# Kernel tuning notes

Hardware: AMD Instinct MI355X
Metric: run time of the kernel (lower is better)

The kernel has to match this reference:

```python
import jax, jax.numpy as jnp
import numpy as np

EPS = 1e-5  # eqx.nn.LayerNorm default


def _layer_norm(x, w, b):
    m = x.mean(-1, keepdims=True)
    v = ((x - m) ** 2).mean(-1, keepdims=True)
    return (x - m) / jnp.sqrt(v + EPS) * w + b


def _s4_block(x, nw, nb, lre, lim, bre, bim, cre, cim, d, lstep, ow, ob, o2w, o2b):
    # x: [L, H]. One SequenceBlock: LayerNorm -> S4 recurrence (lax.scan) -> GELU -> GLU-style gated linear -> residual.
    skip = x
    h = _layer_norm(x, nw, nb)
    Lam = lre + 1j * lim                      # [H, N] complex diagonal state matrix
    step = jnp.exp(lstep)[:, None]            # [H, 1] per-channel timescale
    BL = 1.0 / (1.0 - (step / 2.0) * Lam)     # bilinear discretization
    Abar = BL * (1.0 + (step / 2.0) * Lam)    # [H, N]
    Bbar = BL * step * (bre + 1j * bim)       # [H, N]
    C = cre + 1j * cim                        # [H, N]

    def scan_fn(state, u):                    # state: [H, N] complex, u: [H]
        new = Abar * state + Bbar * u[:, None]
        y = 2.0 * jnp.sum(C * new, axis=-1).real + d * u
        return new, y

    init = jnp.zeros(Abar.shape, Abar.dtype)  # cell.init_state
    _, y = jax.lax.scan(scan_fn, init, h)     # [L, H]
    y = jax.nn.gelu(y)
    y = (y @ ow.T + ob) * jax.nn.sigmoid(y @ o2w.T + o2b)
    return skip + y


def setup_inputs() -> dict:
    key = jax.random.key(0)
    L, IN, OUT, H, N, NL = 2048, 4, 3, 512, 32, 4
    ks = jax.random.split(key, 16)
    return {
        "x": jax.random.normal(ks[0], (L, IN), jnp.float32),
        "enc_w": jax.random.normal(ks[1], (H, IN), jnp.float32) / np.sqrt(IN),
        "enc_b": jnp.zeros((H,), jnp.float32),
        "dec_w": jax.random.normal(ks[2], (OUT, H), jnp.float32) / np.sqrt(H),
        "dec_b": jnp.zeros((OUT,), jnp.float32),
        "norm_w": jnp.ones((NL, H), jnp.float32),
        "norm_b": jnp.zeros((NL, H), jnp.float32),
        "lam_re": -0.5 - jax.random.uniform(ks[3], (NL, H, N), jnp.float32),  # stable (Re < 0)
        "lam_im": np.pi * jax.random.normal(ks[4], (NL, H, N), jnp.float32),
        "b_re": jax.random.normal(ks[5], (NL, H, N), jnp.float32) / np.sqrt(N),
        "b_im": jax.random.normal(ks[6], (NL, H, N), jnp.float32) / np.sqrt(N),
        "c_re": jax.random.normal(ks[7], (NL, H, N), jnp.float32) / np.sqrt(N),
        "c_im": jax.random.normal(ks[8], (NL, H, N), jnp.float32) / np.sqrt(N),
        "d": jax.random.normal(ks[9], (NL, H), jnp.float32),
        "log_step": float(np.log(1e-3)) + float(np.log(1e-1) - np.log(1e-3)) * jax.random.uniform(ks[10], (NL, H), jnp.float32),
        "out_w": jax.random.normal(ks[11], (NL, H, H), jnp.float32) / np.sqrt(H),
        "out_b": jnp.zeros((NL, H), jnp.float32),
        "out2_w": jax.random.normal(ks[12], (NL, H, H), jnp.float32) / np.sqrt(H),
        "out2_b": jnp.zeros((NL, H), jnp.float32),
    }


def reference(x, enc_w, enc_b, dec_w, dec_b, norm_w, norm_b, lam_re, lam_im, b_re, b_im, c_re, c_im, d, log_step, out_w, out_b, out2_w, out2_b):
    h = x @ enc_w.T + enc_b                   # encoder: [L, IN] -> [L, H]
    for i in range(norm_w.shape[0]):          # fixed small n_layers loop
        h = _s4_block(h, norm_w[i], norm_b[i], lam_re[i], lam_im[i], b_re[i], b_im[i],
                      c_re[i], c_im[i], d[i], log_step[i], out_w[i], out_b[i], out2_w[i], out2_b[i])
    return h @ dec_w.T + dec_b                # decoder: [L, H] -> [L, OUT]
```

## Files before the change

### kernel.cpp

```cpp
#include <hip/hip_runtime.h>
#include <hip/hip_bf16.h>
#include <math.h>

#define LSEQ 2048
#define HD   512
#define NST  32
#define LC   64
#define NCHK 32
#define HH   (HD * HD)

typedef __bf16 bf16;
typedef __bf16 bf16x8 __attribute__((ext_vector_type(8)));
typedef float  floatx4 __attribute__((ext_vector_type(4)));

__device__ __forceinline__ float wave_reduce_add(float v) {
#pragma unroll
    for (int m = 32; m; m >>= 1) v += __shfl_xor(v, m, 64);
    return v;
}

__device__ __forceinline__ float gelu_tanh(float x) {
    float z = 0.7978845608028654f * (x + 0.044715f * x * x * x);
    float e = __expf(2.f * z);
    float th = 1.f - 2.f / (e + 1.f);
    return 0.5f * x * (1.f + th);
}

__device__ __forceinline__ void make_ab(float lre, float lim, float step,
                                        float br0, float bi0,
                                        float& ar, float& ai, float& br, float& bi) {
    float s2 = 0.5f * step;
    float dr = 1.f - s2 * lre, di = -s2 * lim;
    float inv = 1.f / (dr * dr + di * di);
    float blr = dr * inv, bli = -di * inv;
    float nr = 1.f + s2 * lre, ni = s2 * lim;
    ar = blr * nr - bli * ni;
    ai = blr * ni + bli * nr;
    float tr = step * br0, ti = step * bi0;
    br = blr * tr - bli * ti;
    bi = blr * ti + bli * tr;
}

__global__ __launch_bounds__(256) void cvt_kernel(
    const float* __restrict__ ow, const float* __restrict__ o2w,
    bf16* __restrict__ wb) {
    const float* src = blockIdx.y ? o2w : ow;
    bf16* dst = wb + blockIdx.y * (4 * HH);
    int i = (blockIdx.x * 256 + threadIdx.x) * 8;
    float4 a = *(const float4*)(src + i);
    float4 b = *(const float4*)(src + i + 4);
    bf16x8 o;
    o[0] = (bf16)a.x; o[1] = (bf16)a.y; o[2] = (bf16)a.z; o[3] = (bf16)a.w;
    o[4] = (bf16)b.x; o[5] = (bf16)b.y; o[6] = (bf16)b.z; o[7] = (bf16)b.w;
    *(bf16x8*)(dst + i) = o;
}

__global__ __launch_bounds__(256) void enc_kernel(
    const float* __restrict__ x, const float* __restrict__ w,
    const float* __restrict__ b, float* __restrict__ h) {
    int idx = blockIdx.x * 256 + threadIdx.x;
    int t = idx >> 9, i = idx & (HD - 1);
    float acc = b[i];
    float4 xv = *(const float4*)(x + t * 4);
    float4 wv = *(const float4*)(w + i * 4);
    acc = fmaf(xv.x, wv.x, acc);
    acc = fmaf(xv.y, wv.y, acc);
    acc = fmaf(xv.z, wv.z, acc);
    acc = fmaf(xv.w, wv.w, acc);
    h[idx] = acc;
}

__global__ __launch_bounds__(256) void ln_kernel(
    const float* __restrict__ h, float* __restrict__ hn,
    const float* __restrict__ w, const float* __restrict__ b) {
    int wv = threadIdx.x >> 6, lane = threadIdx.x & 63;
    int row = blockIdx.x * 4 + wv;
    const float* hp = h + row * HD + lane * 8;
    float v[8];
    *(float4*)(v)     = *(const float4*)(hp);
    *(float4*)(v + 4) = *(const float4*)(hp + 4);
    float s = 0.f;
#pragma unroll
    for (int e = 0; e < 8; ++e) s += v[e];
    s = wave_reduce_add(s);
    float m = s * (1.f / HD);
    float q = 0.f;
#pragma unroll
    for (int e = 0; e < 8; ++e) { float d = v[e] - m; q += d * d; }
    q = wave_reduce_add(q);
    float rstd = rsqrtf(q * (1.f / HD) + 1e-5f);
    float w8[8], b8[8];
    *(float4*)(w8)     = *(const float4*)(w + lane * 8);
    *(float4*)(w8 + 4) = *(const float4*)(w + lane * 8 + 4);
    *(float4*)(b8)     = *(const float4*)(b + lane * 8);
    *(float4*)(b8 + 4) = *(const float4*)(b + lane * 8 + 4);
    float o[8];
#pragma unroll
    for (int e = 0; e < 8; ++e)
        o[e] = (v[e] - m) * rstd * w8[e] + b8[e];
    float* op = hn + row * HD + lane * 8;
    *(float4*)op       = *(float4*)o;
    *(float4*)(op + 4) = *(float4*)(o + 4);
}

__global__ __launch_bounds__(256) void p1_kernel(
    const float* __restrict__ u,
    const float* __restrict__ lre_p, const float* __restrict__ lim_p,
    const float* __restrict__ bre_p, const float* __restrict__ bim_p,
    const float* __restrict__ lstep_p,
    float2* __restrict__ f) {
    int ch = blockIdx.x * 32 + (threadIdx.x >> 3);
    int sub = threadIdx.x & 7;
    int chunk = blockIdx.y;
    float step = __expf(lstep_p[ch]);
    float ar[4], ai[4], br[4], bi[4], sr[4] = {0,0,0,0}, si[4] = {0,0,0,0};
#pragma unroll
    for (int j = 0; j < 4; ++j) {
        int idx = ch * NST + sub + 8 * j;
        make_ab(lre_p[idx], lim_p[idx], step,
                bre_p[idx], bim_p[idx], ar[j], ai[j], br[j], bi[j]);
    }
    const float* up = u + chunk * LC * HD + ch;
#pragma unroll 4
    for (int t = 0; t < LC; ++t) {
        float uu = up[t * HD];
#pragma unroll
        for (int j = 0; j < 4; ++j) {
            float nr = fmaf(ar[j], sr[j], fmaf(-ai[j], si[j], br[j] * uu));
            float ni = fmaf(ai[j], sr[j], fmaf( ar[j], si[j], bi[j] * uu));
            sr[j] = nr; si[j] = ni;
        }
    }
#pragma unroll
    for (int j = 0; j < 4; ++j)
        f[(chunk * HD + ch) * NST + sub + 8 * j] = make_float2(sr[j], si[j]);
}

__global__ __launch_bounds__(256) void p3_kernel(
    const float* __restrict__ u, const float2* __restrict__ f,
    const float* __restrict__ lre_p, const float* __restrict__ lim_p,
    const float* __restrict__ bre_p, const float* __restrict__ bim_p,
    const float* __restrict__ cre_p, const float* __restrict__ cim_p,
    const float* __restrict__ d_p,   const float* __restrict__ lstep_p,
    bf16* __restrict__ g) {
    int ch = blockIdx.x * 32 + (threadIdx.x >> 3);
    int sub = threadIdx.x & 7;
    int chunk = blockIdx.y;
    float step = __expf(lstep_p[ch]);
    float dch = d_p[ch];
    float ar[4], ai[4], br[4], bi[4], cr[4], ci[4];
#pragma unroll
    for (int j = 0; j < 4; ++j) {
        int idx = ch * NST + sub + 8 * j;
        make_ab(lre_p[idx], lim_p[idx], step,
                bre_p[idx], bim_p[idx], ar[j], ai[j], br[j], bi[j]);
        cr[j] = cre_p[idx];
        ci[j] = cim_p[idx];
    }
    float pr[4], pi[4];
#pragma unroll
    for (int j = 0; j < 4; ++j) {
        float xr = ar[j], xi = ai[j];
#pragma unroll
        for (int q = 0; q < 6; ++q) { float tt = xr * xr - xi * xi; xi = 2.f * xr * xi; xr = tt; }
        pr[j] = xr; pi[j] = xi;
    }
    float sr[4] = {0,0,0,0}, si[4] = {0,0,0,0};
    for (int c = 0; c < chunk; ++c) {
#pragma unroll
        for (int j = 0; j < 4; ++j) {
            float2 fv = f[(c * HD + ch) * NST + sub + 8 * j];
            float nr = fmaf(pr[j], sr[j], fmaf(-pi[j], si[j], fv.x));
            float ni = fmaf(pi[j], sr[j], fmaf( pr[j], si[j], fv.y));
            sr[j] = nr; si[j] = ni;
        }
    }
    const float* up = u + chunk * LC * HD + ch;
    bf16* gp = g + chunk * LC * HD + ch;
#pragma unroll 4
    for (int t = 0; t < LC; ++t) {
        float uu = up[t * HD];
        float p = 0.f;
#pragma unroll
        for (int j = 0; j < 4; ++j) {
            float nr = fmaf(ar[j], sr[j], fmaf(-ai[j], si[j], br[j] * uu));
            float ni = fmaf(ai[j], sr[j], fmaf( ar[j], si[j], bi[j] * uu));
            sr[j] = nr; si[j] = ni;
            p = fmaf(cr[j], nr, fmaf(-ci[j], ni, p));
        }
        p += __shfl_xor(p, 1);
        p += __shfl_xor(p, 2);
        p += __shfl_xor(p, 4);
        if (sub == 0) {
            float y = fmaf(dch, uu, 2.f * p);
            gp[t * HD] = (bf16)gelu_tanh(y);
        }
    }
}

__global__ __launch_bounds__(256) void mm_kernel(
    const bf16* __restrict__ A,
    const bf16* __restrict__ W1,
    const bf16* __restrict__ W2,
    const float* __restrict__ bias1, const float* __restrict__ bias2,
    float* __restrict__ Hio) {
    const int w = threadIdx.x >> 6, lane = threadIdx.x & 63;
    const int wm = w >> 1, wn = w & 1;
    const int mBase = blockIdx.y * 64 + wm * 32;
    const int nBase = blockIdx.x * 64 + wn * 32;
    const int lrow = lane & 15, quad = lane >> 4;

    floatx4 acc1[2][2] = {{{0.f,0.f,0.f,0.f},{0.f,0.f,0.f,0.f}},{{0.f,0.f,0.f,0.f},{0.f,0.f,0.f,0.f}}};
    floatx4 acc2[2][2] = {{{0.f,0.f,0.f,0.f},{0.f,0.f,0.f,0.f}},{{0.f,0.f,0.f,0.f},{0.f,0.f,0.f,0.f}}};

    for (int k0 = 0; k0 < HD; k0 += 32) {
        int kk = k0 + quad * 8;
        bf16x8 a0 = *(const bf16x8*)(A + (mBase + lrow) * HD + kk);
        bf16x8 a1 = *(const bf16x8*)(A + (mBase + 16 + lrow) * HD + kk);
        bf16x8 p0 = *(const bf16x8*)(W1 + (nBase + lrow) * HD + kk);
        bf16x8 p1 = *(const bf16x8*)(W1 + (nBase + 16 + lrow) * HD + kk);
        bf16x8 q0 = *(const bf16x8*)(W2 + (nBase + lrow) * HD + kk);
        bf16x8 q1 = *(const bf16x8*)(W2 + (nBase + 16 + lrow) * HD + kk);
        acc1[0][0] = __builtin_amdgcn_mfma_f32_16x16x32_bf16(a0, p0, acc1[0][0], 0, 0, 0);
        acc1[0][1] = __builtin_amdgcn_mfma_f32_16x16x32_bf16(a0, p1, acc1[0][1], 0, 0, 0);
        acc1[1][0] = __builtin_amdgcn_mfma_f32_16x16x32_bf16(a1, p0, acc1[1][0], 0, 0, 0);
        acc1[1][1] = __builtin_amdgcn_mfma_f32_16x16x32_bf16(a1, p1, acc1[1][1], 0, 0, 0);
        acc2[0][0] = __builtin_amdgcn_mfma_f32_16x16x32_bf16(a0, q0, acc2[0][0], 0, 0, 0);
        acc2[0][1] = __builtin_amdgcn_mfma_f32_16x16x32_bf16(a0, q1, acc2[0][1], 0, 0, 0);
        acc2[1][0] = __builtin_amdgcn_mfma_f32_16x16x32_bf16(a1, q0, acc2[1][0], 0, 0, 0);
        acc2[1][1] = __builtin_amdgcn_mfma_f32_16x16x32_bf16(a1, q1, acc2[1][1], 0, 0, 0);
    }

#pragma unroll
    for (int fm = 0; fm < 2; ++fm)
#pragma unroll
        for (int fn = 0; fn < 2; ++fn) {
            int j = nBase + fn * 16 + lrow;
            float bb1 = bias1[j], bb2 = bias2[j];
#pragma unroll
            for (int r = 0; r < 4; ++r) {
                int t = mBase + fm * 16 + quad * 4 + r;
                float z1 = acc1[fm][fn][r] + bb1;
                float z2 = acc2[fm][fn][r] + bb2;
                float val = z1 / (1.f + __expf(-z2));
                Hio[t * HD + j] += val;
            }
        }
}

__global__ __launch_bounds__(192) void dec_kernel(
    const float* __restrict__ h, const float* __restrict__ w,
    const float* __restrict__ b, float* __restrict__ out) {
    int j = threadIdx.x >> 6, lane = threadIdx.x & 63;
    int t = blockIdx.x;
    const float* hp = h + t * HD + lane * 8;
    float v[8];
    *(float4*)(v)     = *(const float4*)(hp);
    *(float4*)(v + 4) = *(const float4*)(hp + 4);
    float w8[8];
    *(float4*)(w8)     = *(const float4*)(w + j * HD + lane * 8);
    *(float4*)(w8 + 4) = *(const float4*)(w + j * HD + lane * 8 + 4);
    float s = 0.f;
#pragma unroll
    for (int e = 0; e < 8; ++e) s = fmaf(v[e], w8[e], s);
    s = wave_reduce_add(s);
    if (lane == 0) out[t * 3 + j] = s + b[j];
}

extern "C" void kernel_launch(void* const* d_in, const int* in_sizes, int n_in,
                              void* d_out, int out_size, void* d_ws, size_t ws_size,
                              hipStream_t stream) {
    const float* x   = (const float*)d_in[0];
    const float* ew  = (const float*)d_in[1];
    const float* eb  = (const float*)d_in[2];
    const float* dw  = (const float*)d_in[3];
    const float* db  = (const float*)d_in[4];
    const float* nw  = (const float*)d_in[5];
    const float* nb  = (const float*)d_in[6];
    const float* lre = (const float*)d_in[7];
    const float* lim = (const float*)d_in[8];
    const float* bre = (const float*)d_in[9];
    const float* bim = (const float*)d_in[10];
    const float* cre = (const float*)d_in[11];
    const float* cim = (const float*)d_in[12];
    const float* dd  = (const float*)d_in[13];
    const float* ls  = (const float*)d_in[14];
    const float* ow  = (const float*)d_in[15];
    const float* ob  = (const float*)d_in[16];
    const float* o2w = (const float*)d_in[17];
    const float* o2b = (const float*)d_in[18];

    char* ws = (char*)d_ws;
    float*  h  = (float*)ws;
    float*  hn = (float*)(ws + (4 << 20));
    float2* f  = (float2*)(ws + (8 << 20));
    bf16*   g  = (bf16*)(ws + (12 << 20));
    bf16*   wb = (bf16*)(ws + (14 << 20));

    cvt_kernel<<<dim3(4 * HH / (256 * 8), 2), 256, 0, stream>>>(ow, o2w, wb);
    enc_kernel<<<LSEQ * HD / 256, 256, 0, stream>>>(x, ew, eb, h);
    for (int lay = 0; lay < 4; ++lay) {
        int oHN = lay * HD * NST, oH = lay * HD;
        ln_kernel<<<LSEQ / 4, 256, 0, stream>>>(h, hn, nw + oH, nb + oH);
        p1_kernel<<<dim3(HD / 32, NCHK), 256, 0, stream>>>(
            hn, lre + oHN, lim + oHN, bre + oHN, bim + oHN, ls + oH, f);
        p3_kernel<<<dim3(HD / 32, NCHK), 256, 0, stream>>>(
            hn, f, lre + oHN, lim + oHN, bre + oHN, bim + oHN,
            cre + oHN, cim + oHN, dd + oH, ls + oH, g);
        mm_kernel<<<dim3(HD / 64, LSEQ / 64), 256, 0, stream>>>(
            g, wb + lay * HH, wb + 4 * HH + lay * HH, ob + oH, o2b + oH, h);
    }
    dec_kernel<<<LSEQ, 192, 0, stream>>>(h, dw, db, (float*)d_out);
}
```

Before: 365.7 us.

## Restructure S4 chunked scan into three passes with precomputed discretized coefficients

The discretized A, B, C and A^16 coefficients for all layers are now computed once by a prep kernel in a channel-major layout, replacing the per-thread recomputation in each scan kernel. The chunked scan becomes three phases with smaller chunks (16 steps, 128 chunks). A new p2 kernel performs a sequential carry scan across chunks, replacing p3's quadratic per-chunk replay of all earlier chunk states. Each thread now holds 16 states, so the cross-lane reduction needs one shuffle, at the cost of higher register pressure and an extra launch per layer.

```diff
diff --git a/kernel.cpp b/kernel.cpp
--- a/kernel.cpp
+++ b/kernel.cpp
@@ -5,8 +5,8 @@
 #define LSEQ 2048
 #define HD   512
 #define NST  32
-#define LC   64
-#define NCHK 32
+#define LC   16
+#define NCHK 128
 #define HH   (HD * HD)
 
 typedef __bf16 bf16;
@@ -41,6 +41,30 @@
     bi = blr * ti + bli * tr;
 }
 
+__global__ __launch_bounds__(256) void prep_kernel(
+    const float* __restrict__ lre, const float* __restrict__ lim,
+    const float* __restrict__ bre, const float* __restrict__ bim,
+    const float* __restrict__ cre, const float* __restrict__ cim,
+    const float* __restrict__ ls,
+    float2* __restrict__ cA, float2* __restrict__ cB,
+    float2* __restrict__ cC, float2* __restrict__ cAp) {
+    int tid = blockIdx.x * 256 + threadIdx.x;
+    int lay = tid >> 14, rem = tid & 16383;
+    int ch = rem >> 5, n = rem & 31;
+    int src = tid;
+    float step = __expf(ls[lay * HD + ch]);
+    float ar, ai, br, bi;
+    make_ab(lre[src], lim[src], step, bre[src], bim[src], ar, ai, br, bi);
+    float xr = ar, xi = ai;
+#pragma unroll
+    for (int q = 0; q < 4; ++q) { float tt = xr * xr - xi * xi; xi = 2.f * xr * xi; xr = tt; }
+    int dst = (lay * NST + n) * HD + ch;
+    cA[dst]  = make_float2(ar, ai);
+    cB[dst]  = make_float2(br, bi);
+    cC[dst]  = make_float2(2.f * cre[src], 2.f * cim[src]);
+    cAp[dst] = make_float2(xr, xi);
+}
+
 __global__ __launch_bounds__(256) void cvt_kernel(
     const float* __restrict__ ow, const float* __restrict__ o2w,
     bf16* __restrict__ wb) {
@@ -103,77 +127,83 @@
     *(float4*)(op + 4) = *(float4*)(o + 4);
 }
 
-__global__ __launch_bounds__(256) void p1_kernel(
+__global__ __launch_bounds__(256, 1) void p1_kernel(
     const float* __restrict__ u,
-    const float* __restrict__ lre_p, const float* __restrict__ lim_p,
-    const float* __restrict__ bre_p, const float* __restrict__ bim_p,
-    const float* __restrict__ lstep_p,
-    float2* __restrict__ f) {
-    int ch = blockIdx.x * 32 + (threadIdx.x >> 3);
-    int sub = threadIdx.x & 7;
-    int chunk = blockIdx.y;
-    float step = __expf(lstep_p[ch]);
-    float ar[4], ai[4], br[4], bi[4], sr[4] = {0,0,0,0}, si[4] = {0,0,0,0};
-#pragma unroll
-    for (int j = 0; j < 4; ++j) {
-        int idx = ch * NST + sub + 8 * j;
-        make_ab(lre_p[idx], lim_p[idx], step,
-                bre_p[idx], bim_p[idx], ar[j], ai[j], br[j], bi[j]);
-    }
+    const float2* __restrict__ cA, const float2* __restrict__ cB,
+    float2* __restrict__ f, int lay) {
+    int lane = threadIdx.x & 63, w = threadIdx.x >> 6;
+    int ch = blockIdx.x * 32 + (lane & 31);
+    int sub = lane >> 5;
+    int chunk = blockIdx.y * 4 + w;
+    int cbase = (lay * NST + sub * 16) * HD + ch;
+    float aR[16], aI[16], bR[16], bI[16];
+#pragma unroll
+    for (int j = 0; j < 16; ++j) {
+        float2 t = cA[cbase + j * HD]; aR[j] = t.x; aI[j] = t.y;
+        t = cB[cbase + j * HD];        bR[j] = t.x; bI[j] = t.y;
+    }
+    float sr[16], si[16];
+#pragma unroll
+    for (int j = 0; j < 16; ++j) { sr[j] = 0.f; si[j] = 0.f; }
     const float* up = u + chunk * LC * HD + ch;
 #pragma unroll 4
     for (int t = 0; t < LC; ++t) {
         float uu = up[t * HD];
 #pragma unroll
-        for (int j = 0; j < 4; ++j) {
-            float nr = fmaf(ar[j], sr[j], fmaf(-ai[j], si[j], br[j] * uu));
-            float ni = fmaf(ai[j], sr[j], fmaf( ar[j], si[j], bi[j] * uu));
+        for (int j = 0; j < 16; ++j) {
+            float nr = fmaf(aR[j], sr[j], fmaf(-aI[j], si[j], bR[j] * uu));
+            float ni = fmaf(aI[j], sr[j], fmaf( aR[j], si[j], bI[j] * uu));
             sr[j] = nr; si[j] = ni;
         }
     }
-#pragma unroll
-    for (int j = 0; j < 4; ++j)
-        f[(chunk * HD + ch) * NST + sub + 8 * j] = make_float2(sr[j], si[j]);
-}
-
-__global__ __launch_bounds__(256) void p3_kernel(
+    float2* fp = f + (chunk * NST + sub * 16) * HD + ch;
+#pragma unroll
+    for (int j = 0; j < 16; ++j) fp[j * HD] = make_float2(sr[j], si[j]);
+}
+
+__global__ __launch_bounds__(64, 1) void p2_kernel(
+    float2* __restrict__ f, const float2* __restrict__ cAp, int lay) {
+    int ch = blockIdx.x * 64 + threadIdx.x;
+    int n = blockIdx.y;
+    float2 ap = cAp[(lay * NST + n) * HD + ch];
+    float sr = 0.f, si = 0.f;
+    float2* fp = f + n * HD + ch;
+#pragma unroll 4
+    for (int c = 0; c < NCHK; ++c) {
+        float2 v = fp[(size_t)c * NST * HD];
+        float nr = fmaf(ap.x, sr, fmaf(-ap.y, si, v.x));
+        float ni = fmaf(ap.y, sr, fmaf( ap.x, si, v.y));
+        sr = nr; si = ni;
+        fp[(size_t)c * NST * HD] = make_float2(sr, si);
+    }
+}
+
+__global__ __launch_bounds__(256, 1) void p3_kernel(
     const float* __restrict__ u, const float2* __restrict__ f,
-    const float* __restrict__ lre_p, const float* __restrict__ lim_p,
-    const float* __restrict__ bre_p, const float* __restrict__ bim_p,
-    const float* __restrict__ cre_p, const float* __restrict__ cim_p,
-    const float* __restrict__ d_p,   const float* __restrict__ lstep_p,
-    bf16* __restrict__ g) {
-    int ch = blockIdx.x * 32 + (threadIdx.x >> 3);
-    int sub = threadIdx.x & 7;
-    int chunk = blockIdx.y;
-    float step = __expf(lstep_p[ch]);
-    float dch = d_p[ch];
-    float ar[4], ai[4], br[4], bi[4], cr[4], ci[4];
-#pragma unroll
-    for (int j = 0; j < 4; ++j) {
-        int idx = ch * NST + sub + 8 * j;
-        make_ab(lre_p[idx], lim_p[idx], step,
-                bre_p[idx], bim_p[idx], ar[j], ai[j], br[j], bi[j]);
-        cr[j] = cre_p[idx];
-        ci[j] = cim_p[idx];
-    }
-    float pr[4], pi[4];
-#pragma unroll
-    for (int j = 0; j < 4; ++j) {
-        float xr = ar[j], xi = ai[j];
-#pragma unroll
-        for (int q = 0; q < 6; ++q) { float tt = xr * xr - xi * xi; xi = 2.f * xr * xi; xr = tt; }
-        pr[j] = xr; pi[j] = xi;
-    }
-    float sr[4] = {0,0,0,0}, si[4] = {0,0,0,0};
-    for (int c = 0; c < chunk; ++c) {
-#pragma unroll
-        for (int j = 0; j < 4; ++j) {
-            float2 fv = f[(c * HD + ch) * NST + sub + 8 * j];
-            float nr = fmaf(pr[j], sr[j], fmaf(-pi[j], si[j], fv.x));
-            float ni = fmaf(pi[j], sr[j], fmaf( pr[j], si[j], fv.y));
-            sr[j] = nr; si[j] = ni;
-        }
+    const float2* __restrict__ cA, const float2* __restrict__ cB,
+    const float2* __restrict__ cC, const float* __restrict__ d_p,
+    bf16* __restrict__ g, int lay) {
+    int lane = threadIdx.x & 63, w = threadIdx.x >> 6;
+    int ch = blockIdx.x * 32 + (lane & 31);
+    int sub = lane >> 5;
+    int chunk = blockIdx.y * 4 + w;
+    int cbase = (lay * NST + sub * 16) * HD + ch;
+    float aR[16], aI[16], bR[16], bI[16], cR[16], cI[16];
+#pragma unroll
+    for (int j = 0; j < 16; ++j) {
+        float2 t = cA[cbase + j * HD]; aR[j] = t.x; aI[j] = t.y;
+        t = cB[cbase + j * HD];        bR[j] = t.x; bI[j] = t.y;
+        t = cC[cbase + j * HD];        cR[j] = t.x; cI[j] = t.y;
+    }
+    float dch = d_p[lay * HD + ch];
+    float sr[16], si[16];
+    if (chunk > 0) {
+        const float2* ip = f + ((chunk - 1) * NST + sub * 16) * HD + ch;
+#pragma unroll
+        for (int j = 0; j < 16; ++j) { float2 v = ip[j * HD]; sr[j] = v.x; si[j] = v.y; }
+    } else {
+#pragma unroll
+        for (int j = 0; j < 16; ++j) { sr[j] = 0.f; si[j] = 0.f; }
     }
     const float* up = u + chunk * LC * HD + ch;
     bf16* gp = g + chunk * LC * HD + ch;
@@ -182,19 +212,15 @@
         float uu = up[t * HD];
         float p = 0.f;
 #pragma unroll
-        for (int j = 0; j < 4; ++j) {
-            float nr = fmaf(ar[j], sr[j], fmaf(-ai[j], si[j], br[j] * uu));
-            float ni = fmaf(ai[j], sr[j], fmaf( ar[j], si[j], bi[j] * uu));
+        for (int j = 0; j < 16; ++j) {
+            float nr = fmaf(aR[j], sr[j], fmaf(-aI[j], si[j], bR[j] * uu));
+            float ni = fmaf(aI[j], sr[j], fmaf( aR[j], si[j], bI[j] * uu));
             sr[j] = nr; si[j] = ni;
-            p = fmaf(cr[j], nr, fmaf(-ci[j], ni, p));
+            p = fmaf(cR[j], nr, fmaf(-cI[j], ni, p));
         }
-        p += __shfl_xor(p, 1);
-        p += __shfl_xor(p, 2);
-        p += __shfl_xor(p, 4);
-        if (sub == 0) {
-            float y = fmaf(dch, uu, 2.f * p);
-            gp[t * HD] = (bf16)gelu_tanh(y);
-        }
+        p += __shfl_xor(p, 32);
+        float y = fmaf(dch, uu, p);
+        if (sub == 0) gp[t * HD] = (bf16)gelu_tanh(y);
     }
 }
 
@@ -291,22 +317,25 @@
     const float* o2b = (const float*)d_in[18];
 
     char* ws = (char*)d_ws;
-    float*  h  = (float*)ws;
-    float*  hn = (float*)(ws + (4 << 20));
-    float2* f  = (float2*)(ws + (8 << 20));
-    bf16*   g  = (bf16*)(ws + (12 << 20));
-    bf16*   wb = (bf16*)(ws + (14 << 20));
-
+    float*  h   = (float*)ws;
+    float*  hn  = (float*)(ws + (4  << 20));
+    float2* f   = (float2*)(ws + (8  << 20));
+    bf16*   g   = (bf16*)(ws + (24 << 20));
+    bf16*   wb  = (bf16*)(ws + (26 << 20));
+    float2* cA  = (float2*)(ws + (30 << 20));
+    float2* cB  = (float2*)(ws + (30 << 20) + (512 << 10));
+    float2* cC  = (float2*)(ws + (31 << 20));
+    float2* cAp = (float2*)(ws + (31 << 20) + (512 << 10));
+
+    prep_kernel<<<256, 256, 0, stream>>>(lre, lim, bre, bim, cre, cim, ls, cA, cB, cC, cAp);
     cvt_kernel<<<dim3(4 * HH / (256 * 8), 2), 256, 0, stream>>>(ow, o2w, wb);
     enc_kernel<<<LSEQ * HD / 256, 256, 0, stream>>>(x, ew, eb, h);
     for (int lay = 0; lay < 4; ++lay) {
-        int oHN = lay * HD * NST, oH = lay * HD;
+        int oH = lay * HD;
         ln_kernel<<<LSEQ / 4, 256, 0, stream>>>(h, hn, nw + oH, nb + oH);
-        p1_kernel<<<dim3(HD / 32, NCHK), 256, 0, stream>>>(
-            hn, lre + oHN, lim + oHN, bre + oHN, bim + oHN, ls + oH, f);
-        p3_kernel<<<dim3(HD / 32, NCHK), 256, 0, stream>>>(
-            hn, f, lre + oHN, lim + oHN, bre + oHN, bim + oHN,
-            cre + oHN, cim + oHN, dd + oH, ls + oH, g);
+        p1_kernel<<<dim3(HD / 32, NCHK / 4), 256, 0, stream>>>(hn, cA, cB, f, lay);
+        p2_kernel<<<dim3(HD / 64, NST), 64, 0, stream>>>(f, cAp, lay);
+        p3_kernel<<<dim3(HD / 32, NCHK / 4), 256, 0, stream>>>(hn, f, cA, cB, cC, dd, g, lay);
         mm_kernel<<<dim3(HD / 64, LSEQ / 64), 256, 0, stream>>>(
             g, wb + lay * HH, wb + 4 * HH + lay * HH, ob + oH, o2b + oH, h);
     }
```

Result: faster. 351.0 us (-4.0%).
